# Optimization experiments

Hardware: AMD Instinct MI355X
Metric: run time of the kernel (lower is better)

The kernel has to match this reference:

```python
import jax, jax.numpy as jnp
import numpy as np

ALPHA = 0.2          # LeakyReLU negative slope
BN_EPS = 1e-5
NEG_INF = -9e15


def setup_inputs() -> dict:
    key = jax.random.key(0)
    k1, k2, k3, k4 = jax.random.split(key, 4)
    B, N, Fin, Fout = 4, 4096, 64, 64
    h = jax.random.normal(k1, (B, N, Fin), dtype=jnp.float32)
    adj = jax.random.randint(k2, (N, N), 0, 2, dtype=jnp.int32)
    # xavier_uniform with gain 1.414
    gain = 1.414
    bW = gain * np.sqrt(6.0 / (Fin + Fout))
    W = jax.random.uniform(k3, (Fin, Fout), dtype=jnp.float32, minval=-bW, maxval=bW)
    ba = gain * np.sqrt(6.0 / (2 * Fout + 1))
    a = jax.random.uniform(k4, (2 * Fout, 1), dtype=jnp.float32, minval=-ba, maxval=ba)
    gamma = jnp.ones((N,), dtype=jnp.float32)
    beta = jnp.zeros((N,), dtype=jnp.float32)
    return {"h": h, "adj": adj, "W": W, "a": a, "gamma": gamma, "beta": beta}


def reference(h, adj, W, a, gamma, beta):
    # h: [B,N,Fin], adj: [N,N], W: [Fin,Fout], a: [2*Fout,1]
    N = adj.shape[0]
    Fout = W.shape[1]
    dk = jnp.asarray(N, h.dtype) ** 0.5
    Wh = jnp.einsum('bnf,fo->bno', h, W)                # [B,N,Fout]
    Wh1 = Wh @ a[:Fout]                                 # [B,N,1]
    Wh2 = Wh @ a[Fout:]                                 # [B,N,1]
    e = (Wh1 + jnp.swapaxes(Wh2, 1, 2)) / dk            # [B,N,N] broadcast add
    e = jax.nn.leaky_relu(e, negative_slope=ALPHA)
    scores = jnp.where(adj[None] > 0, e, NEG_INF)
    attention = jax.nn.softmax(scores, axis=2)          # dropout is identity at inference
    h_prime = jnp.einsum('bij,bjo->bio', attention, Wh) # [B,N,Fout]
    # BatchNorm1d(N): channel axis is the node axis, normalize over (B, Fout)
    mean = h_prime.mean(axis=(0, 2), keepdims=True)
    var = h_prime.var(axis=(0, 2), keepdims=True)
    h_prime = gamma[None, :, None] * (h_prime - mean) * jax.lax.rsqrt(var + BN_EPS) + beta[None, :, None]
    out = h_prime + h                                   # in==out -> res_net is None
    return jax.nn.elu(out)                              # concat=True
```

## Files before the change

### kernel.cpp

```cpp
#include <hip/hip_runtime.h>
#include <hip/hip_fp16.h>
#include <math.h>

#define NN 4096
#define SCL 0.022542110013890054f
#define LOG2E 1.4426950408889634f

typedef __attribute__((ext_vector_type(8))) _Float16 f16x8;
typedef __attribute__((ext_vector_type(2))) _Float16 f16x2;
typedef __attribute__((ext_vector_type(4))) float f32x4;
typedef __attribute__((ext_vector_type(4))) short s16x4;

__device__ __forceinline__ float exp2_fast(float x) {
  float r; asm("v_exp_f32 %0, %1" : "=v"(r) : "v"(x)); return r;
}
__device__ __forceinline__ unsigned short h16(float x) {
  _Float16 h = (_Float16)x; return *(unsigned short*)&h;
}

__global__ __launch_bounds__(256)
void k_prep(const float* __restrict__ h, const float* __restrict__ W,
            const float* __restrict__ a, const int* __restrict__ adj,
            unsigned short* __restrict__ WhTf, unsigned* __restrict__ Ei1,
            unsigned* __restrict__ Ei2, unsigned* __restrict__ Ej1,
            unsigned* __restrict__ Ej2, unsigned* __restrict__ bits) {
  __shared__ float sW[4096];
  __shared__ unsigned short T[64][8];
  const int t = threadIdx.x;
  const int bi = blockIdx.x;
  const int q2 = bi >> 1;
  if ((bi & 1) == 0) {
    const int w = t >> 6, lane = t & 63;
    const int hr = q2 * 4 + w;
    const int r = hr >> 1, half = hr & 1;
    const int kq = lane >> 1, hi = lane & 1;
    const int* __restrict__ src = adj + ((size_t)r << 12) + half * 2048;
    int v[32];
#pragma unroll
    for (int k = 0; k < 32; ++k) v[k] = src[k * 64 + lane];
    unsigned myw = 0;
#pragma unroll
    for (int k = 0; k < 32; ++k) {
      unsigned long long m = __ballot(v[k] != 0);
      unsigned lohi = hi ? (unsigned)(m >> 32) : (unsigned)m;
      myw = (kq == k) ? lohi : myw;
    }
    bits[((size_t)r << 7) + half * 64 + lane] = myw;
    return;
  }
#pragma unroll
  for (int i = 0; i < 16; ++i) sW[i * 256 + t] = W[i * 256 + t];
  __syncthreads();
  const int wv = t >> 6, lane = t & 63;
  const float a1 = a[lane], a2 = a[64 + lane];
  const int row0 = q2 * 8;
  const int q0 = row0 + wv * 2;
  float w1v[2], w2v[2];
  for (int r = 0; r < 2; ++r) {
    const int row = q0 + r;
    const float* hr = h + (size_t)row * 64;
    float acc = 0.f;
#pragma unroll
    for (int k = 0; k < 64; ++k) acc = fmaf(hr[k], sW[k * 64 + lane], acc);
    T[lane][wv * 2 + r] = h16(acc);
    float r1 = acc * a1, r2 = acc * a2;
#pragma unroll
    for (int sft = 32; sft; sft >>= 1) { r1 += __shfl_xor(r1, sft); r2 += __shfl_xor(r2, sft); }
    w1v[r] = r1 * SCL; w2v[r] = r2 * SCL;
  }
  if (lane == 0) {
#pragma unroll
    for (int r = 0; r < 2; ++r) {
      unsigned u1 = h16(exp2_fast(w1v[r]));
      unsigned u2 = h16(exp2_fast(0.2f * w1v[r]));
      Ei1[q0 + r] = u1 | (u1 << 16);
      Ei2[q0 + r] = u2 | (u2 << 16);
    }
    Ej1[q0 >> 1] = (unsigned)h16(exp2_fast(w2v[0])) |
                   ((unsigned)h16(exp2_fast(w2v[1])) << 16);
    Ej2[q0 >> 1] = (unsigned)h16(exp2_fast(0.2f * w2v[0])) |
                   ((unsigned)h16(exp2_fast(0.2f * w2v[1])) << 16);
  }
  __syncthreads();
  const int f = t >> 2, jp4 = t & 3;
  const int b = row0 >> 12, n0 = row0 & 4095;
  const int g32 = n0 >> 5, rgq = (n0 >> 3) & 3;
  unsigned v = *(unsigned*)&T[f][jp4 * 2];
  unsigned short* dst = WhTf +
      ((((size_t)(b * 4 + (f >> 4)) << 7) + g32) << 9) +
      ((rgq * 16 + (f & 15)) << 3) + jp4 * 2;
  *(unsigned*)dst = v;
}

__global__ __launch_bounds__(512, 2)
void k_gat(const unsigned* __restrict__ bits,
           const unsigned short* __restrict__ WhTf,
           const unsigned* __restrict__ Ei1, const unsigned* __restrict__ Ei2,
           const unsigned* __restrict__ Ej1, const unsigned* __restrict__ Ej2,
           unsigned short* __restrict__ Pp, float* __restrict__ lsp) {
  __shared__ unsigned mlds[256][17];

  const int t = threadIdx.x;
  const int w = t >> 6, lane = t & 63;
  const int jp = lane & 15, rg = lane >> 4;
  const int bid = blockIdx.x;
  const int c = bid >> 6;
  const int b = (bid >> 4) & 3;
  const int i0b = (bid & 15) * 256;
  const int i0 = i0b + w * 32;
  const int g0 = c * 16;

#pragma unroll
  for (int pass = 0; pass < 8; ++pass) {
    const int row = pass * 32 + (t >> 4);
    mlds[row][t & 15] = bits[((size_t)(i0b + row) << 7) + g0 + (t & 15)];
  }

  unsigned ei1u[2], ei2u[2];
#pragma unroll
  for (int il = 0; il < 2; ++il) {
    ei1u[il] = Ei1[b * NN + i0 + il * 16 + jp];
    ei2u[il] = Ei2[b * NN + i0 + il * 16 + jp];
  }
  const unsigned short* __restrict__ abase =
      WhTf + (((size_t)(b * 4) << 7) + g0) * 512 + lane * 8;
  const unsigned* __restrict__ ej1b = Ej1 + (b << 11) + (g0 << 4) + (rg << 2);
  const unsigned* __restrict__ ej2b = Ej2 + (b << 11) + (g0 << 4) + (rg << 2);

  f32x4 acc[2][4];
  f32x4 accd[2];
#pragma unroll
  for (int il = 0; il < 2; ++il) {
    accd[il] = (f32x4){0.f, 0.f, 0.f, 0.f};
#pragma unroll
    for (int ft = 0; ft < 4; ++ft) acc[il][ft] = (f32x4){0.f, 0.f, 0.f, 0.f};
  }
  f16x8 ones;
#pragma unroll
  for (int e = 0; e < 8; ++e) ones[e] = (_Float16)1.0f;

  __syncthreads();

#pragma unroll 4
  for (int jt = 0; jt < 16; ++jt) {
    const f16x8 af0 = *(const f16x8*)(abase + (0 * 128 + jt) * 512);
    const f16x8 af1 = *(const f16x8*)(abase + (1 * 128 + jt) * 512);
    const f16x8 af2 = *(const f16x8*)(abase + (2 * 128 + jt) * 512);
    const f16x8 af3 = *(const f16x8*)(abase + (3 * 128 + jt) * 512);
    const uint4 e1p = *(const uint4*)(ej1b + jt * 16);
    const uint4 e2p = *(const uint4*)(ej2b + jt * 16);
    const unsigned e1a[4] = {e1p.x, e1p.y, e1p.z, e1p.w};
    const unsigned e2a[4] = {e2p.x, e2p.y, e2p.z, e2p.w};

    f16x8 pf[2];
#pragma unroll
    for (int il = 0; il < 2; ++il) {
      const unsigned mb = mlds[w * 32 + il * 16 + jp][jt] >> (rg * 8);
      const f16x2 x1 = *(const f16x2*)&ei1u[il];
      const f16x2 x2 = *(const f16x2*)&ei2u[il];
      unsigned pw[4];
#pragma unroll
      for (int p4 = 0; p4 < 4; ++p4) {
        f16x2 c1 = x1 * (*(const f16x2*)&e1a[p4]);
        f16x2 c2 = x2 * (*(const f16x2*)&e2a[p4]);
        f16x2 mx = __builtin_elementwise_max(c1, c2);
        unsigned mexp = (((mb >> (2 * p4)) & 1u) ? 0xFFFFu : 0u) |
                        (((mb >> (2 * p4 + 1)) & 1u) ? 0xFFFF0000u : 0u);
        pw[p4] = (*(unsigned*)&mx) & mexp;
      }
      pf[il] = *(f16x8*)pw;
    }
#pragma unroll
    for (int il = 0; il < 2; ++il) {
      accd[il] = __builtin_amdgcn_mfma_f32_16x16x32_f16(ones, pf[il], accd[il], 0, 0, 0);
      acc[il][0] = __builtin_amdgcn_mfma_f32_16x16x32_f16(af0, pf[il], acc[il][0], 0, 0, 0);
      acc[il][1] = __builtin_amdgcn_mfma_f32_16x16x32_f16(af1, pf[il], acc[il][1], 0, 0, 0);
      acc[il][2] = __builtin_amdgcn_mfma_f32_16x16x32_f16(af2, pf[il], acc[il][2], 0, 0, 0);
      acc[il][3] = __builtin_amdgcn_mfma_f32_16x16x32_f16(af3, pf[il], acc[il][3], 0, 0, 0);
    }
  }

  if (rg == 0) {
#pragma unroll
    for (int il = 0; il < 2; ++il)
      lsp[(size_t)(c * 4 + b) * NN + i0 + il * 16 + jp] = accd[il][0];
  }
  const size_t pbase = (((size_t)(c * 4 + b)) * NN + i0) * 64;
#pragma unroll
  for (int il = 0; il < 2; ++il)
#pragma unroll
    for (int ft = 0; ft < 4; ++ft) {
      s16x4 pk;
#pragma unroll
      for (int r = 0; r < 4; ++r) pk[r] = (short)h16(acc[il][ft][r]);
      *(s16x4*)(Pp + pbase + (size_t)(il * 16 + jp) * 64 + ft * 16 + rg * 4) = pk;
    }
}

__global__ __launch_bounds__(256)
void k_bn(const float* __restrict__ h, const unsigned short* __restrict__ Pp,
          const float* __restrict__ lsp, const float* __restrict__ gamma,
          const float* __restrict__ beta, float* __restrict__ out) {
  __shared__ float bnp[8][4][2];
  const int t = threadIdx.x;
  const int w = t >> 6, lane = t & 63;
  const int nl = lane >> 3, fs = lane & 7;
  const int i = blockIdx.x * 8 + nl;

  float xa[8] = {0.f, 0.f, 0.f, 0.f, 0.f, 0.f, 0.f, 0.f};
  float lt = 0.f;
#pragma unroll
  for (int cc = 0; cc < 8; ++cc) {
    const size_t base = ((size_t)(cc * 4 + w) * NN + i);
    f16x8 v = *(const f16x8*)(Pp + base * 64 + fs * 8);
#pragma unroll
    for (int k = 0; k < 8; ++k) xa[k] += (float)v[k];
    lt += lsp[base];
  }
  const float invl = 1.f / lt;
  float s1 = 0.f, s2 = 0.f;
#pragma unroll
  for (int k = 0; k < 8; ++k) {
    xa[k] *= invl;
    s1 += xa[k]; s2 += xa[k] * xa[k];
  }
  s1 += __shfl_xor(s1, 1); s2 += __shfl_xor(s2, 1);
  s1 += __shfl_xor(s1, 2); s2 += __shfl_xor(s2, 2);
  s1 += __shfl_xor(s1, 4); s2 += __shfl_xor(s2, 4);
  if (fs == 0) { bnp[nl][w][0] = s1; bnp[nl][w][1] = s2; }
  __syncthreads();
  const float t1 = bnp[nl][0][0] + bnp[nl][1][0] + bnp[nl][2][0] + bnp[nl][3][0];
  const float t2 = bnp[nl][0][1] + bnp[nl][1][1] + bnp[nl][2][1] + bnp[nl][3][1];
  const float mean = t1 * (1.f / 256.f);
  const float var  = t2 * (1.f / 256.f) - mean * mean;
  const float sc = gamma[i] * rsqrtf(var + 1e-5f);
  const float bt = beta[i];
  const size_t off = (((size_t)(w * NN + i)) << 6) + fs * 8;
  const float4 hv0 = *(const float4*)(h + off);
  const float4 hv1 = *(const float4*)(h + off + 4);
  const float hvv[8] = {hv0.x, hv0.y, hv0.z, hv0.w, hv1.x, hv1.y, hv1.z, hv1.w};
  float o[8];
#pragma unroll
  for (int k = 0; k < 8; ++k) {
    float v = sc * (xa[k] - mean) + bt + hvv[k];
    o[k] = v > 0.f ? v : exp2_fast(v * LOG2E) - 1.f;
  }
  *(float4*)(out + off)     = make_float4(o[0], o[1], o[2], o[3]);
  *(float4*)(out + off + 4) = make_float4(o[4], o[5], o[6], o[7]);
}

extern "C" void kernel_launch(void* const* d_in, const int* in_sizes, int n_in,
                              void* d_out, int out_size, void* d_ws, size_t ws_size,
                              hipStream_t stream) {
  (void)in_sizes; (void)n_in; (void)out_size; (void)ws_size;
  const float* h     = (const float*)d_in[0];
  const int*   adj   = (const int*)d_in[1];
  const float* W     = (const float*)d_in[2];
  const float* a     = (const float*)d_in[3];
  const float* gamma = (const float*)d_in[4];
  const float* beta  = (const float*)d_in[5];
  float* out = (float*)d_out;

  char* ws = (char*)d_ws;
  unsigned short* WhTf = (unsigned short*)ws;
  unsigned* bits = (unsigned*)(ws + (2u << 20));
  unsigned* Ei1 = (unsigned*)(ws + (4u << 20));
  unsigned* Ei2 = (unsigned*)(ws + (4u << 20) + (64u << 10));
  unsigned* Ej1 = (unsigned*)(ws + (4u << 20) + (128u << 10));
  unsigned* Ej2 = (unsigned*)(ws + (4u << 20) + (160u << 10));
  float* lsp = (float*)(ws + (4u << 20) + (192u << 10));
  unsigned short* Pp = (unsigned short*)(ws + (5u << 20));

  k_prep<<<4096, 256, 0, stream>>>(h, W, a, adj, WhTf, Ei1, Ei2, Ej1, Ej2, bits);
  k_gat<<<512, 512, 0, stream>>>(bits, WhTf, Ei1, Ei2, Ej1, Ej2, Pp, lsp);
  k_bn<<<512, 256, 0, stream>>>(h, Pp, lsp, gamma, beta, out);
}
```

Baseline: 51.33 us.

## Fuse adjacency mask packing into attention kernel with batch-shared byte mask in LDS

Removes the bitmask-packing half of the prep kernel and has the attention kernel load the int32 adjacency directly, converting it to a byte mask in shared memory. Blocks are remapped so each covers 64 rows across all four batches, letting one mask tile serve every batch. This drops the intermediate bitmask write/read and a serial stage, at the cost of a larger LDS footprint and a heavy global-load prologue in the compute kernel.

```diff
diff --git a/kernel.cpp b/kernel.cpp
--- a/kernel.cpp
+++ b/kernel.cpp
@@ -20,40 +20,19 @@
 
 __global__ __launch_bounds__(256)
 void k_prep(const float* __restrict__ h, const float* __restrict__ W,
-            const float* __restrict__ a, const int* __restrict__ adj,
-            unsigned short* __restrict__ WhTf, unsigned* __restrict__ Ei1,
-            unsigned* __restrict__ Ei2, unsigned* __restrict__ Ej1,
-            unsigned* __restrict__ Ej2, unsigned* __restrict__ bits) {
+            const float* __restrict__ a, unsigned short* __restrict__ WhTf,
+            unsigned* __restrict__ Ei1, unsigned* __restrict__ Ei2,
+            unsigned* __restrict__ Ej1, unsigned* __restrict__ Ej2) {
   __shared__ float sW[4096];
   __shared__ unsigned short T[64][8];
   const int t = threadIdx.x;
   const int bi = blockIdx.x;
-  const int q2 = bi >> 1;
-  if ((bi & 1) == 0) {
-    const int w = t >> 6, lane = t & 63;
-    const int hr = q2 * 4 + w;
-    const int r = hr >> 1, half = hr & 1;
-    const int kq = lane >> 1, hi = lane & 1;
-    const int* __restrict__ src = adj + ((size_t)r << 12) + half * 2048;
-    int v[32];
-#pragma unroll
-    for (int k = 0; k < 32; ++k) v[k] = src[k * 64 + lane];
-    unsigned myw = 0;
-#pragma unroll
-    for (int k = 0; k < 32; ++k) {
-      unsigned long long m = __ballot(v[k] != 0);
-      unsigned lohi = hi ? (unsigned)(m >> 32) : (unsigned)m;
-      myw = (kq == k) ? lohi : myw;
-    }
-    bits[((size_t)r << 7) + half * 64 + lane] = myw;
-    return;
-  }
 #pragma unroll
   for (int i = 0; i < 16; ++i) sW[i * 256 + t] = W[i * 256 + t];
   __syncthreads();
   const int wv = t >> 6, lane = t & 63;
   const float a1 = a[lane], a2 = a[64 + lane];
-  const int row0 = q2 * 8;
+  const int row0 = bi * 8;
   const int q0 = row0 + wv * 2;
   float w1v[2], w2v[2];
   for (int r = 0; r < 2; ++r) {
@@ -93,27 +72,44 @@
 }
 
 __global__ __launch_bounds__(512, 2)
-void k_gat(const unsigned* __restrict__ bits,
+void k_gat(const int* __restrict__ adj,
            const unsigned short* __restrict__ WhTf,
            const unsigned* __restrict__ Ei1, const unsigned* __restrict__ Ei2,
            const unsigned* __restrict__ Ej1, const unsigned* __restrict__ Ej2,
            unsigned short* __restrict__ Pp, float* __restrict__ lsp) {
-  __shared__ unsigned mlds[256][17];
+  __shared__ unsigned char m8[64][520];
 
   const int t = threadIdx.x;
   const int w = t >> 6, lane = t & 63;
   const int jp = lane & 15, rg = lane >> 4;
   const int bid = blockIdx.x;
   const int c = bid >> 6;
-  const int b = (bid >> 4) & 3;
-  const int i0b = (bid & 15) * 256;
-  const int i0 = i0b + w * 32;
+  const int i0b = (bid & 63) * 64;
+  const int b = w >> 1, ih = w & 1;
+  const int i0 = i0b + ih * 32;
   const int g0 = c * 16;
 
-#pragma unroll
-  for (int pass = 0; pass < 8; ++pass) {
-    const int row = pass * 32 + (t >> 4);
-    mlds[row][t & 15] = bits[((size_t)(i0b + row) << 7) + g0 + (t & 15)];
+  {
+    const int rl = t >> 7;
+    const int cb = (t & 127) * 4;
+    const int* __restrict__ src =
+        adj + (((size_t)(i0b + rl)) << 12) + c * 512 + cb;
+#pragma unroll
+    for (int half = 0; half < 2; ++half) {
+      int4 va[8];
+#pragma unroll
+      for (int p = 0; p < 8; ++p)
+        va[p] = *(const int4*)(src + (((size_t)(half * 32 + p * 4)) << 12));
+#pragma unroll
+      for (int p = 0; p < 8; ++p) {
+        const int row = half * 32 + p * 4 + rl;
+        unsigned pk = (unsigned)(va[p].x != 0) |
+                      ((unsigned)(va[p].y != 0) << 8) |
+                      ((unsigned)(va[p].z != 0) << 16) |
+                      ((unsigned)(va[p].w != 0) << 24);
+        *(unsigned*)&m8[row][cb] = pk;
+      }
+    }
   }
 
   unsigned ei1u[2], ei2u[2];
@@ -155,7 +151,8 @@
     f16x8 pf[2];
 #pragma unroll
     for (int il = 0; il < 2; ++il) {
-      const unsigned mb = mlds[w * 32 + il * 16 + jp][jt] >> (rg * 8);
+      const unsigned long long mv = *(const unsigned long long*)
+          &m8[ih * 32 + il * 16 + jp][jt * 32 + rg * 8];
       const f16x2 x1 = *(const f16x2*)&ei1u[il];
       const f16x2 x2 = *(const f16x2*)&ei2u[il];
       unsigned pw[4];
@@ -164,8 +161,8 @@
         f16x2 c1 = x1 * (*(const f16x2*)&e1a[p4]);
         f16x2 c2 = x2 * (*(const f16x2*)&e2a[p4]);
         f16x2 mx = __builtin_elementwise_max(c1, c2);
-        unsigned mexp = (((mb >> (2 * p4)) & 1u) ? 0xFFFFu : 0u) |
-                        (((mb >> (2 * p4 + 1)) & 1u) ? 0xFFFF0000u : 0u);
+        unsigned mexp = (((mv >> (16 * p4)) & 0xFFull) ? 0xFFFFu : 0u) |
+                        (((mv >> (16 * p4 + 8)) & 0xFFull) ? 0xFFFF0000u : 0u);
         pw[p4] = (*(unsigned*)&mx) & mexp;
       }
       pf[il] = *(f16x8*)pw;
@@ -263,7 +260,6 @@
 
   char* ws = (char*)d_ws;
   unsigned short* WhTf = (unsigned short*)ws;
-  unsigned* bits = (unsigned*)(ws + (2u << 20));
   unsigned* Ei1 = (unsigned*)(ws + (4u << 20));
   unsigned* Ei2 = (unsigned*)(ws + (4u << 20) + (64u << 10));
   unsigned* Ej1 = (unsigned*)(ws + (4u << 20) + (128u << 10));
@@ -271,7 +267,7 @@
   float* lsp = (float*)(ws + (4u << 20) + (192u << 10));
   unsigned short* Pp = (unsigned short*)(ws + (5u << 20));
 
-  k_prep<<<4096, 256, 0, stream>>>(h, W, a, adj, WhTf, Ei1, Ei2, Ej1, Ej2, bits);
-  k_gat<<<512, 512, 0, stream>>>(bits, WhTf, Ei1, Ei2, Ej1, Ej2, Pp, lsp);
+  k_prep<<<2048, 256, 0, stream>>>(h, W, a, WhTf, Ei1, Ei2, Ej1, Ej2);
+  k_gat<<<512, 512, 0, stream>>>(adj, WhTf, Ei1, Ei2, Ej1, Ej2, Pp, lsp);
   k_bn<<<512, 256, 0, stream>>>(h, Pp, lsp, gamma, beta, out);
 }
```

After: 55.21 us. 7.6% more time.
